# Optimization experiments

Hardware: AMD Instinct MI355X
Metric: run time of the kernel (lower is better)

## Reference

```python
import jax, jax.numpy as jnp
import numpy as np

B, D, T = 8, 1024, 512
HID, NH, NL = 256, 4, 2
OUT = HID // NH  # 64 per-head dim
ALPHA = 0.2      # leaky relu slope
EPS = 1e-5       # layernorm eps


def setup_inputs() -> dict:
    key = jax.random.key(0)
    ks = jax.random.split(key, 10)
    X_obs = jax.random.normal(ks[0], (B, D, T), dtype=jnp.float32)
    mask = (jax.random.uniform(ks[1], (B, D, T)) < 0.8).astype(jnp.float32)
    W_in = jax.random.normal(ks[2], (2 * T, HID), dtype=jnp.float32) * (1.0 / np.sqrt(2 * T))
    b_in = jnp.zeros((HID,), dtype=jnp.float32)
    gat_W = jax.random.normal(ks[3], (NL, NH, HID, OUT), dtype=jnp.float32) * (1.0 / np.sqrt(HID))
    gat_a = jax.random.normal(ks[4], (NL, NH, 2 * OUT), dtype=jnp.float32) * 0.1
    ln_g = jnp.ones((NL, HID), dtype=jnp.float32)
    ln_b = jnp.zeros((NL, HID), dtype=jnp.float32)
    W_out = jax.random.normal(ks[5], (HID, T), dtype=jnp.float32) * (1.0 / np.sqrt(HID))
    b_out = jnp.zeros((T,), dtype=jnp.float32)
    return dict(X_obs=X_obs, mask=mask, W_in=W_in, b_in=b_in, gat_W=gat_W,
                gat_a=gat_a, ln_g=ln_g, ln_b=ln_b, W_out=W_out, b_out=b_out)


def _layer_norm(x, g, b):
    mu = jnp.mean(x, axis=-1, keepdims=True)
    var = jnp.mean((x - mu) ** 2, axis=-1, keepdims=True)
    return (x - mu) * jax.lax.rsqrt(var + EPS) * g + b


def _gat_forward(X_obs, mask, W_in, b_in, gat_W, gat_a, ln_g, ln_b, W_out, b_out):
    # mean-impute per (d, t) position across batch
    obs_sum = jnp.sum(X_obs * mask, axis=0, keepdims=True)
    obs_cnt = jnp.sum(mask, axis=0, keepdims=True)
    pos_mean = obs_sum / (obs_cnt + 1e-10)
    X_mean = X_obs * mask + (1.0 - mask) * pos_mean

    x = jnp.concatenate([X_mean, mask], axis=-1)       # (B, D, 2T)
    h = x @ W_in + b_in                                 # (B, N, HID)

    for l in range(NL):
        Wl = gat_W[l]                                   # (H, HID, OUT)
        a_left = gat_a[l, :, :OUT]                      # (H, OUT)
        a_right = gat_a[l, :, OUT:]                     # (H, OUT)
        hW = jnp.einsum('bnd,hde->bhne', h, Wl)         # (B, H, N, OUT)
        # e_ij = leakyrelu(a_left . h_i + a_right . h_j) -- avoids O(N^2 * 2d) concat
        s_l = jnp.einsum('bhne,he->bhn', hW, a_left)
        s_r = jnp.einsum('bhne,he->bhn', hW, a_right)
        e = jax.nn.leaky_relu(s_l[..., :, None] + s_r[..., None, :], ALPHA)  # (B,H,N,N)
        attn = jax.nn.softmax(e, axis=-1)
        head_out = jnp.einsum('bhnm,bhme->bhne', attn, hW)                   # (B,H,N,OUT)
        h_new = jnp.transpose(head_out, (0, 2, 1, 3)).reshape(h.shape[0], h.shape[1], HID)
        h = _layer_norm(h + h_new, ln_g[l], ln_b[l])

    return h @ W_out + b_out                            # (B, D, T)


def reference(X_obs, mask, W_in, b_in, gat_W, gat_a, ln_g, ln_b, W_out, b_out):
    return _gat_forward(X_obs, mask, W_in, b_in, gat_W, gat_a, ln_g, ln_b, W_out, b_out)
```

## Files before the change

### kernel.cpp

```cpp
#include <hip/hip_runtime.h>
#include <hip/hip_bf16.h>

constexpr int B_   = 8;
constexpr int D_   = 1024;
constexpr int T_   = 512;
constexpr int HID_ = 256;
constexpr int NH_  = 4;
constexpr int NL_  = 2;
constexpr float ALPHA_ = 0.2f;
constexpr float EPS_   = 1e-5f;
constexpr int OUT_ = 64;
constexpr int M_ = B_ * D_;
constexpr int DT_ = D_ * T_;
constexpr int KIN_ = 2 * T_;
constexpr int CKS_ = 132;
constexpr int NCH_ = 32;
constexpr int CR_  = 32;

typedef __attribute__((ext_vector_type(8))) short short8;
typedef __attribute__((ext_vector_type(4))) float floatx4;

__device__ __forceinline__ unsigned short f2bf(float f) {
    unsigned int u = __float_as_uint(f);
    unsigned int r = u + 0x7fffu + ((u >> 16) & 1u);
    return (unsigned short)(r >> 16);
}
__device__ __forceinline__ float bf2f(unsigned short u) {
    return __uint_as_float(((unsigned int)u) << 16);
}
__device__ __forceinline__ unsigned int kenc(float f) {
    unsigned int u = __float_as_uint(f);
    return (u & 0x80000000u) ? ~u : (u | 0x80000000u);
}
__device__ __forceinline__ float kdec(unsigned int k) {
    unsigned int u = (k & 0x80000000u) ? (k ^ 0x80000000u) : ~k;
    return __uint_as_float(u);
}

__global__ __launch_bounds__(256) void prep_k(const float* __restrict__ X,
                                              const float* __restrict__ Mk,
                                              const float* __restrict__ W_in,
                                              const float* __restrict__ gatW,
                                              const float* __restrict__ W_out,
                                              unsigned short* __restrict__ Ain,
                                              unsigned short* __restrict__ Wt_in,
                                              unsigned short* __restrict__ Wcat,
                                              unsigned short* __restrict__ WtO,
                                              unsigned int* __restrict__ rmaxkey) {
    int bx = blockIdx.x;
    if (bx < 512) {
        int idx4 = (bx * 256 + threadIdx.x) * 4;
        int t = idx4 & (T_ - 1);
        int d = idx4 >> 9;
        float4 x[B_], m[B_];
        float4 s = {0, 0, 0, 0}, c = {0, 0, 0, 0};
#pragma unroll
        for (int b = 0; b < B_; b++) {
            x[b] = *(const float4*)&X[(size_t)b * DT_ + idx4];
            m[b] = *(const float4*)&Mk[(size_t)b * DT_ + idx4];
            s.x += x[b].x * m[b].x; s.y += x[b].y * m[b].y;
            s.z += x[b].z * m[b].z; s.w += x[b].w * m[b].w;
            c.x += m[b].x; c.y += m[b].y; c.z += m[b].z; c.w += m[b].w;
        }
        float4 pm;
        pm.x = s.x / (c.x + 1e-10f); pm.y = s.y / (c.y + 1e-10f);
        pm.z = s.z / (c.z + 1e-10f); pm.w = s.w / (c.w + 1e-10f);
#pragma unroll
        for (int b = 0; b < B_; b++) {
            size_t row = (size_t)b * D_ + d;
            ushort4 xm, mk;
            xm.x = f2bf(x[b].x * m[b].x + (1.f - m[b].x) * pm.x);
            xm.y = f2bf(x[b].y * m[b].y + (1.f - m[b].y) * pm.y);
            xm.z = f2bf(x[b].z * m[b].z + (1.f - m[b].z) * pm.z);
            xm.w = f2bf(x[b].w * m[b].w + (1.f - m[b].w) * pm.w);
            mk.x = f2bf(m[b].x); mk.y = f2bf(m[b].y);
            mk.z = f2bf(m[b].z); mk.w = f2bf(m[b].w);
            *(ushort4*)&Ain[row * KIN_ + t]      = xm;
            *(ushort4*)&Ain[row * KIN_ + T_ + t] = mk;
        }
    } else {
        int idx = (bx - 512) * 256 + threadIdx.x;
        if (idx < 64) rmaxkey[idx] = 0u;
        if (idx < 262144) {
            int n = idx >> 10, k = idx & 1023;
            Wt_in[idx] = f2bf(W_in[(size_t)k * HID_ + n]);
        } else if (idx < 393216) {
            int j = idx - 262144;
            int l = j >> 16, n = (j >> 8) & 255, k = j & 255;
            int h = n >> 6, e = n & 63;
            Wcat[j] = f2bf(gatW[(((size_t)(l * NH_ + h) * HID_) + k) * OUT_ + e]);
        } else {
            int j = idx - 393216;
            int n = j >> 8, k = j & 255;
            WtO[j] = f2bf(W_out[(size_t)k * T_ + n]);
        }
    }
}

template <int MODE>
__global__ __launch_bounds__(256) void gemm_bf16_k(
        const unsigned short* __restrict__ A,
        const unsigned short* __restrict__ Bt,
        const float* __restrict__ bias,
        float* __restrict__ C,
        unsigned short* __restrict__ Cb,
        const float* __restrict__ ga,
        float* __restrict__ s_l,
        float* __restrict__ s_r,
        unsigned int* __restrict__ rmaxkey,
        int Nsz, int Ksz) {
    __shared__ __align__(16) unsigned short As[2][64 * 72];
    __shared__ __align__(16) unsigned short Bs[2][64 * 72];
    int tid = threadIdx.x;
    int wave = tid >> 6, lane = tid & 63;
    int q = lane >> 4, r16 = lane & 15;
    int rowbase = blockIdx.y * 64;
    int colbase = blockIdx.x * 64;

    int srow = tid >> 3, sk = (tid & 7) * 8;
    const unsigned short* Ap0 = A + (size_t)(rowbase + srow) * Ksz + sk;
    const unsigned short* Ap1 = A + (size_t)(rowbase + srow + 32) * Ksz + sk;
    const unsigned short* Bp0 = Bt + (size_t)(colbase + srow) * Ksz + sk;
    const unsigned short* Bp1 = Bt + (size_t)(colbase + srow + 32) * Ksz + sk;
    int la0 = srow * 72 + sk, la1 = (srow + 32) * 72 + sk;

    floatx4 acc[4];
#pragma unroll
    for (int i = 0; i < 4; i++) acc[i] = (floatx4)0.f;

    uint4 pa0 = *(const uint4*)Ap0, pa1 = *(const uint4*)Ap1;
    uint4 pb0 = *(const uint4*)Bp0, pb1 = *(const uint4*)Bp1;
    *(uint4*)&As[0][la0] = pa0;
    *(uint4*)&As[0][la1] = pa1;
    *(uint4*)&Bs[0][la0] = pb0;
    *(uint4*)&Bs[0][la1] = pb1;

    int nk = Ksz >> 6;
    for (int it = 0; it < nk; it++) {
        int cur = it & 1;
        __syncthreads();
        if (it + 1 < nk) {
            int kt = (it + 1) << 6;
            pa0 = *(const uint4*)(Ap0 + kt);
            pa1 = *(const uint4*)(Ap1 + kt);
            pb0 = *(const uint4*)(Bp0 + kt);
            pb1 = *(const uint4*)(Bp1 + kt);
        }
#pragma unroll
        for (int t = 0; t < 2; t++) {
            short8 a = *(const short8*)&As[cur][(wave * 16 + r16) * 72 + t * 32 + q * 8];
#pragma unroll
            for (int ni = 0; ni < 4; ni++) {
                short8 b = *(const short8*)&Bs[cur][(ni * 16 + r16) * 72 + t * 32 + q * 8];
                acc[ni] = __builtin_amdgcn_mfma_f32_16x16x32_bf16(a, b, acc[ni], 0, 0, 0);
            }
        }
        if (it + 1 < nk) {
            int nxt = cur ^ 1;
            *(uint4*)&As[nxt][la0] = pa0;
            *(uint4*)&As[nxt][la1] = pa1;
            *(uint4*)&Bs[nxt][la0] = pb0;
            *(uint4*)&Bs[nxt][la1] = pb1;
        }
    }
    if constexpr (MODE == 2) {
        int bhh = ((rowbase >> 10) << 2) + blockIdx.x;
        int nb0 = rowbase & (D_ - 1);
        int nb = nb0 + wave * 16;
        const float* gab = ga + blockIdx.x * 2 * OUT_;
        float al4[4], ar4[4];
#pragma unroll
        for (int ni = 0; ni < 4; ni++) {
            al4[ni] = gab[ni * 16 + r16];
            ar4[ni] = gab[OUT_ + ni * 16 + r16];
        }
        float slv[4], srv[4];
#pragma unroll
        for (int rr = 0; rr < 4; rr++) {
            float s1 = 0.f, s2 = 0.f;
#pragma unroll
            for (int ni = 0; ni < 4; ni++) {
                s1 += acc[ni][rr] * al4[ni];
                s2 += acc[ni][rr] * ar4[ni];
            }
            slv[rr] = s1;
            srv[rr] = s2;
        }
#pragma unroll
        for (int off = 1; off < 16; off <<= 1) {
#pragma unroll
            for (int rr = 0; rr < 4; rr++) {
                slv[rr] += __shfl_xor(slv[rr], off, 64);
                srv[rr] += __shfl_xor(srv[rr], off, 64);
            }
        }
        {
            int rsel = r16 & 3;
            float sv = (rsel == 0) ? slv[0] : (rsel == 1) ? slv[1] : (rsel == 2) ? slv[2] : slv[3];
            float rv = (rsel == 0) ? srv[0] : (rsel == 1) ? srv[1] : (rsel == 2) ? srv[2] : srv[3];
            int n = nb + q * 4 + rsel;
            if (r16 < 4)                 s_l[bhh * D_ + n] = sv;
            else if (r16 >= 8 && r16 < 12) s_r[bhh * D_ + n] = rv;
        }
        float mx = fmaxf(fmaxf(srv[0], srv[1]), fmaxf(srv[2], srv[3]));
        mx = fmaxf(mx, __shfl_xor(mx, 16, 64));
        mx = fmaxf(mx, __shfl_xor(mx, 32, 64));
        if (lane == 0) atomicMax(&rmaxkey[bhh], kenc(mx));
        __syncthreads();
        unsigned short* st = &As[0][0];
#pragma unroll
        for (int ni = 0; ni < 4; ni++)
#pragma unroll
            for (int rr = 0; rr < 4; rr++)
                st[(wave * 16 + q * 4 + rr) * 72 + ni * 16 + r16] = f2bf(acc[ni][rr]);
        __syncthreads();
#pragma unroll
        for (int i = 0; i < 2; i++) {
            int idx = tid * 2 + i;
            int row = idx >> 3, seg = idx & 7;
            uint4 v = *(const uint4*)&st[row * 72 + seg * 8];
            *(uint4*)&Cb[((size_t)bhh << 16) + ((size_t)(nb0 + row) << 6) + seg * 8] = v;
        }
    } else {
#pragma unroll
        for (int rr = 0; rr < 4; rr++) {
            int row = rowbase + wave * 16 + q * 4 + rr;
#pragma unroll
            for (int ni = 0; ni < 4; ni++) {
                int col = colbase + ni * 16 + r16;
                float v = acc[ni][rr] + (bias ? bias[col] : 0.f);
                C[(size_t)row * Nsz + col] = v;
                if constexpr (MODE == 1) Cb[(size_t)row * Nsz + col] = f2bf(v);
            }
        }
    }
}

__global__ __launch_bounds__(1024) void rank_k(
        const float* __restrict__ sr_g,
        const unsigned int* __restrict__ rmaxkey,
        float* __restrict__ srt,
        int* __restrict__ sig,
        float* __restrict__ wm) {
    __shared__ float skey[1024];
    __shared__ short part[16][64];
    int bh = blockIdx.x, seg = blockIdx.y;
    int tid = threadIdx.x;
    skey[tid] = sr_g[bh * D_ + tid];
    __syncthreads();
    int lane = tid & 63, wv = tid >> 6;
    int el = seg * 64 + lane;
    float k = skey[el];
    int m0 = wv * 64;
    int cnt = 0;
#pragma unroll 4
    for (int m = m0; m < m0 + 64; ++m) {
        float km = skey[m];
        cnt += (km < k) || (km == k && m < el);
    }
    part[wv][lane] = (short)cnt;
    __syncthreads();
    if (tid < 64) {
        int rank = 0;
#pragma unroll
        for (int w = 0; w < 16; ++w) rank += part[w][tid];
        int elg = seg * 64 + tid;
        float key = skey[elg];
        float rm = kdec(rmaxkey[bh]);
        float u = key - rm;
        float w1 = __expf(u), w2 = __expf(ALPHA_ * u);
        srt[bh * D_ + rank] = key;
        sig[bh * D_ + rank] = elg;
        *(float2*)&wm[(size_t)(bh * D_ + rank) * 2] = float2{w1, w2};
    }
}

__global__ __launch_bounds__(64) void chunksum_k(
        const unsigned short* __restrict__ hwN,
        const int* __restrict__ sig,
        const float* __restrict__ wm,
        float* __restrict__ csum,
        float* __restrict__ csca) {
    int bh = blockIdx.x, c = blockIdx.y;
    int e = threadIdx.x;
    const unsigned short* vb = hwN + ((size_t)bh << 16);
    int t0 = c * CR_;
    float a1 = 0.f, a2 = 0.f, q1 = 0.f, q2 = 0.f;
#pragma unroll 4
    for (int t = t0; t < t0 + CR_; ++t) {
        float2 ww = *(const float2*)&wm[(size_t)(bh * D_ + t) * 2];
        float v = bf2f(vb[((size_t)sig[bh * D_ + t] << 6) + e]);
        a1 = fmaf(ww.x, v, a1);
        a2 = fmaf(ww.y, v, a2);
        q1 += ww.x; q2 += ww.y;
    }
    *(float2*)&csum[(((size_t)bh * NCH_ + c) * 64 + e) * 2] = float2{a1, a2};
    if (e == 0) *(float2*)&csca[((size_t)bh * NCH_ + c) * 2] = float2{q1, q2};
}

__global__ __launch_bounds__(64) void ckwrite_k(
        const unsigned short* __restrict__ hwN,
        const int* __restrict__ sig,
        const float* __restrict__ wm,
        const float* __restrict__ csum,
        const float* __restrict__ csca,
        float* __restrict__ ck) {
    int bh = blockIdx.x, c = blockIdx.y;
    int e = threadIdx.x;
    float r1 = 0.f, r2 = 0.f, p1 = 0.f, p2 = 0.f;
    for (int cc = 0; cc < c; ++cc) {
        float2 s  = *(const float2*)&csum[(((size_t)bh * NCH_ + cc) * 64 + e) * 2];
        float2 sc = *(const float2*)&csca[((size_t)bh * NCH_ + cc) * 2];
        r1 += s.x; r2 += s.y;
        p1 += sc.x; p2 += sc.y;
    }
    const unsigned short* vb = hwN + ((size_t)bh << 16);
    float* ckb = ck + (size_t)bh * 1025 * CKS_;
    int t0 = c * CR_;
    for (int t = t0; t < t0 + CR_; ++t) {
        *(float2*)&ckb[(size_t)t * CKS_ + 2 * e] = float2{r1, r2};
        if (e == 0) *(float2*)&ckb[(size_t)t * CKS_ + 128] = float2{p1, p2};
        float2 ww = *(const float2*)&wm[(size_t)(bh * D_ + t) * 2];
        float v = bf2f(vb[((size_t)sig[bh * D_ + t] << 6) + e]);
        r1 = fmaf(ww.x, v, r1);
        r2 = fmaf(ww.y, v, r2);
        p1 += ww.x; p2 += ww.y;
    }
    if (c == NCH_ - 1) {
        *(float2*)&ckb[(size_t)1024 * CKS_ + 2 * e] = float2{r1, r2};
        if (e == 0) *(float2*)&ckb[(size_t)1024 * CKS_ + 128] = float2{p1, p2};
    }
}

__global__ __launch_bounds__(512) void rowln_k(
        float* __restrict__ h,
        const float* __restrict__ sl_g,
        const unsigned int* __restrict__ rmaxkey,
        const float* __restrict__ srt,
        const float* __restrict__ ck,
        const float* __restrict__ g,
        const float* __restrict__ bb,
        unsigned short* __restrict__ hbf) {
    __shared__ float srtL[4][1024];
    __shared__ float hnew[32][260];
    __shared__ float ckT1[4][64];
    __shared__ float qTs[4][2];
    __shared__ float pdF[128][2];
    __shared__ int   pdT[128];
    int blk = blockIdx.x;
    int b = blk >> 5;
    int d0 = (blk & 31) << 5;
    int tid = threadIdx.x;
    for (int i = tid; i < 4096; i += 512)
        srtL[i >> 10][i & 1023] = srt[(size_t)((b * 4 + (i >> 10)) * D_) + (i & 1023)];
    if (tid < 256) {
        int hh = tid >> 6, e = tid & 63;
        ckT1[hh][e] = ck[((size_t)((b * 4 + hh) * 1025 + 1024)) * CKS_ + 2 * e];
    }
    if (tid < 8) {
        int hh = tid >> 1;
        qTs[hh][tid & 1] = ck[((size_t)((b * 4 + hh) * 1025 + 1024)) * CKS_ + 128 + (tid & 1)];
    }
    __syncthreads();
    if (tid < 128) {
        int r = tid & 31, h4 = tid >> 5;
        int bh = b * 4 + h4;
        float sl = sl_g[bh * D_ + d0 + r];
        float rm = kdec(rmaxkey[bh]);
        float x = sl + rm;
        float Mn = fmaxf(x, ALPHA_ * x);
        float A  = __expf(x - Mn);
        float B2 = __expf(ALPHA_ * x - Mn);
        float key = -sl;
        int lo = 0, hi = 1024;
        while (lo < hi) {
            int mid = (lo + hi) >> 1;
            if (srtL[h4][mid] < key) lo = mid + 1; else hi = mid;
        }
        float2 qs = *(const float2*)&ck[((size_t)(bh * 1025 + lo)) * CKS_ + 128];
        float den = A * (qTs[h4][0] - qs.x) + B2 * qs.y;
        float inv = 1.f / den;
        pdF[tid][0] = A * inv;
        pdF[tid][1] = B2 * inv;
        pdT[tid] = lo;
    }
    __syncthreads();
    int wv = tid >> 6, e = tid & 63;
    for (int p = wv; p < 128; p += 8) {
        int r = p & 31, h4 = p >> 5;
        int bh = b * 4 + h4;
        float fA = pdF[p][0], fB = pdF[p][1];
        int t = pdT[p];
        float2 P = *(const float2*)&ck[((size_t)(bh * 1025 + t)) * CKS_ + 2 * e];
        hnew[r][h4 * 64 + e] = fA * (ckT1[h4][e] - P.x) + fB * P.y;
    }
    __syncthreads();
    for (int rr = wv * 4; rr < wv * 4 + 4; ++rr) {
        size_t grow = ((((size_t)b << 10) + d0 + rr) << 8);
        float4 a  = *(const float4*)&h[grow + e * 4];
        float4 nv = *(const float4*)&hnew[rr][e * 4];
        float4 v = {a.x + nv.x, a.y + nv.y, a.z + nv.z, a.w + nv.w};
        float s = v.x + v.y + v.z + v.w;
#pragma unroll
        for (int off = 1; off < 64; off <<= 1) s += __shfl_xor(s, off, 64);
        float mu = s * (1.f / HID_);
        float4 dd = {v.x - mu, v.y - mu, v.z - mu, v.w - mu};
        float s2 = dd.x * dd.x + dd.y * dd.y + dd.z * dd.z + dd.w * dd.w;
#pragma unroll
        for (int off = 1; off < 64; off <<= 1) s2 += __shfl_xor(s2, off, 64);
        float rs = rsqrtf(s2 * (1.f / HID_) + EPS_);
        float4 gg = *(const float4*)&g[e * 4];
        float4 bv = *(const float4*)&bb[e * 4];
        float4 res;
        res.x = dd.x * rs * gg.x + bv.x;
        res.y = dd.y * rs * gg.y + bv.y;
        res.z = dd.z * rs * gg.z + bv.z;
        res.w = dd.w * rs * gg.w + bv.w;
        *(float4*)&h[grow + e * 4] = res;
        ushort4 pk = {f2bf(res.x), f2bf(res.y), f2bf(res.z), f2bf(res.w)};
        *(ushort4*)&hbf[grow + e * 4] = pk;
    }
}

extern "C" void kernel_launch(void* const* d_in, const int* in_sizes, int n_in,
                              void* d_out, int out_size, void* d_ws, size_t ws_size,
                              hipStream_t stream) {
    const float* X_obs = (const float*)d_in[0];
    const float* mask  = (const float*)d_in[1];
    const float* W_in  = (const float*)d_in[2];
    const float* b_in  = (const float*)d_in[3];
    const float* gat_W = (const float*)d_in[4];
    const float* gat_a = (const float*)d_in[5];
    const float* ln_g  = (const float*)d_in[6];
    const float* ln_b  = (const float*)d_in[7];
    const float* W_out = (const float*)d_in[8];
    const float* b_out = (const float*)d_in[9];
    float* out = (float*)d_out;

    char* base = (char*)d_ws;
    unsigned short* Ain = (unsigned short*)base;
    unsigned short* hwN = (unsigned short*)base;
    float* ck   = (float*)(base + (4u << 20));
    float* csum = (float*)(base + (21u << 20));
    float* csca = (float*)(base + (21u << 20) + (512u << 10));
    float* wm   = (float*)(base + (22u << 20));
    float* srtb = (float*)(base + (22u << 20) + (512u << 10));
    int*   sig  = (int*)(base + (22u << 20) + (768u << 10));
    float* hbuf = (float*)(base + (23u << 20));
    unsigned short* hbf   = (unsigned short*)(base + (31u << 20));
    unsigned short* Wt_in = (unsigned short*)(base + (35u << 20));
    unsigned short* Wcat  = Wt_in + (size_t)HID_ * KIN_;
    unsigned short* WtO   = Wcat + (size_t)NL_ * HID_ * HID_;
    float* slb = (float*)(WtO + (size_t)T_ * HID_);
    float* srb = slb + B_ * NH_ * D_;
    unsigned int* rmaxkey = (unsigned int*)(srb + B_ * NH_ * D_);

    prep_k<<<2560, 256, 0, stream>>>(X_obs, mask, W_in, gat_W, W_out,
                                     Ain, Wt_in, Wcat, WtO, rmaxkey);

    gemm_bf16_k<1><<<dim3(HID_ / 64, M_ / 64), 256, 0, stream>>>(
        Ain, Wt_in, b_in, hbuf, hbf, nullptr, nullptr, nullptr, nullptr,
        HID_, KIN_);

    for (int l = 0; l < NL_; l++) {
        gemm_bf16_k<2><<<dim3(HID_ / 64, M_ / 64), 256, 0, stream>>>(
            hbf, Wcat + (size_t)l * HID_ * HID_, nullptr, nullptr, hwN,
            gat_a + (size_t)l * NH_ * 2 * OUT_, slb, srb, rmaxkey + l * 32,
            HID_, HID_);
        rank_k<<<dim3(32, 16), 1024, 0, stream>>>(srb, rmaxkey + l * 32,
                                                  srtb, sig, wm);
        chunksum_k<<<dim3(32, NCH_), 64, 0, stream>>>(hwN, sig, wm, csum, csca);
        ckwrite_k<<<dim3(32, NCH_), 64, 0, stream>>>(hwN, sig, wm, csum, csca, ck);
        rowln_k<<<256, 512, 0, stream>>>(hbuf, slb, rmaxkey + l * 32,
                                         srtb, ck,
                                         ln_g + (size_t)l * HID_,
                                         ln_b + (size_t)l * HID_, hbf);
    }

    gemm_bf16_k<0><<<dim3(T_ / 64, M_ / 64), 256, 0, stream>>>(
        hbf, WtO, b_out, out, nullptr, nullptr, nullptr, nullptr, nullptr,
        T_, HID_);
}
```

Baseline: 249.2 us.

## Fuse all stages into one persistent kernel with software grid barriers

Replaces the sequence of separate launches (prep, input GEMM, per-layer GAT GEMM, rank, chunk-sum, prefix write, row layernorm, output GEMM) with one persistent 512-block kernel. Stages are separated by atomic grid barriers, and each stage's work is remapped onto the fixed block grid. The chunking is also re-split into 64 chunks of 16 rows. This aims to remove launch gaps and tail effects between many small kernels. In exchange it depends on all 512 blocks being co-resident, and some stages now run with fewer threads per block than before.

```diff
diff --git a/kernel.cpp b/kernel.cpp
--- a/kernel.cpp
+++ b/kernel.cpp
@@ -14,8 +14,9 @@
 constexpr int DT_ = D_ * T_;
 constexpr int KIN_ = 2 * T_;
 constexpr int CKS_ = 132;
-constexpr int NCH_ = 32;
-constexpr int CR_  = 32;
+constexpr int NCH_ = 64;
+constexpr int CR_  = 16;
+constexpr int NB_  = 512;
 
 typedef __attribute__((ext_vector_type(8))) short short8;
 typedef __attribute__((ext_vector_type(4))) float floatx4;
@@ -37,19 +38,192 @@
     return __uint_as_float(u);
 }
 
-__global__ __launch_bounds__(256) void prep_k(const float* __restrict__ X,
-                                              const float* __restrict__ Mk,
-                                              const float* __restrict__ W_in,
-                                              const float* __restrict__ gatW,
-                                              const float* __restrict__ W_out,
-                                              unsigned short* __restrict__ Ain,
-                                              unsigned short* __restrict__ Wt_in,
-                                              unsigned short* __restrict__ Wcat,
-                                              unsigned short* __restrict__ WtO,
-                                              unsigned int* __restrict__ rmaxkey) {
-    int bx = blockIdx.x;
-    if (bx < 512) {
-        int idx4 = (bx * 256 + threadIdx.x) * 4;
+__device__ __forceinline__ void gridbar(unsigned int* bar) {
+    __syncthreads();
+    if (threadIdx.x == 0) {
+        __threadfence();
+        atomicAdd(bar, 1u);
+        while (__hip_atomic_load(bar, __ATOMIC_ACQUIRE, __HIP_MEMORY_SCOPE_AGENT)
+               < (unsigned)NB_)
+            __builtin_amdgcn_s_sleep(2);
+    }
+    __syncthreads();
+}
+
+__global__ __launch_bounds__(256) void init_k(unsigned int* __restrict__ bar) {
+    if (threadIdx.x < 64) bar[threadIdx.x] = 0u;
+}
+
+struct GemmSm {
+    unsigned short As[2][64 * 72];
+    unsigned short Bs[2][64 * 72];
+};
+
+template <int MODE>
+__device__ void gemm_tile(
+        const unsigned short* __restrict__ A,
+        const unsigned short* __restrict__ Bt,
+        const float* __restrict__ bias,
+        float* __restrict__ C,
+        unsigned short* __restrict__ Cb,
+        const float* __restrict__ ga,
+        float* __restrict__ s_l,
+        float* __restrict__ s_r,
+        unsigned int* __restrict__ rmaxkey,
+        int Nsz, int Ksz, int bx, int by, GemmSm& sm) {
+    __syncthreads();
+    int tid = threadIdx.x;
+    int wave = tid >> 6, lane = tid & 63;
+    int q = lane >> 4, r16 = lane & 15;
+    int rowbase = by * 64;
+    int colbase = bx * 64;
+
+    int srow = tid >> 3, sk = (tid & 7) * 8;
+    const unsigned short* Ap0 = A + (size_t)(rowbase + srow) * Ksz + sk;
+    const unsigned short* Ap1 = A + (size_t)(rowbase + srow + 32) * Ksz + sk;
+    const unsigned short* Bp0 = Bt + (size_t)(colbase + srow) * Ksz + sk;
+    const unsigned short* Bp1 = Bt + (size_t)(colbase + srow + 32) * Ksz + sk;
+    int la0 = srow * 72 + sk, la1 = (srow + 32) * 72 + sk;
+
+    floatx4 acc[4];
+#pragma unroll
+    for (int i = 0; i < 4; i++) acc[i] = (floatx4)0.f;
+
+    uint4 pa0 = *(const uint4*)Ap0, pa1 = *(const uint4*)Ap1;
+    uint4 pb0 = *(const uint4*)Bp0, pb1 = *(const uint4*)Bp1;
+    *(uint4*)&sm.As[0][la0] = pa0;
+    *(uint4*)&sm.As[0][la1] = pa1;
+    *(uint4*)&sm.Bs[0][la0] = pb0;
+    *(uint4*)&sm.Bs[0][la1] = pb1;
+
+    int nk = Ksz >> 6;
+    for (int it = 0; it < nk; it++) {
+        int cur = it & 1;
+        __syncthreads();
+        if (it + 1 < nk) {
+            int kt = (it + 1) << 6;
+            pa0 = *(const uint4*)(Ap0 + kt);
+            pa1 = *(const uint4*)(Ap1 + kt);
+            pb0 = *(const uint4*)(Bp0 + kt);
+            pb1 = *(const uint4*)(Bp1 + kt);
+        }
+#pragma unroll
+        for (int t = 0; t < 2; t++) {
+            short8 a = *(const short8*)&sm.As[cur][(wave * 16 + r16) * 72 + t * 32 + q * 8];
+#pragma unroll
+            for (int ni = 0; ni < 4; ni++) {
+                short8 b = *(const short8*)&sm.Bs[cur][(ni * 16 + r16) * 72 + t * 32 + q * 8];
+                acc[ni] = __builtin_amdgcn_mfma_f32_16x16x32_bf16(a, b, acc[ni], 0, 0, 0);
+            }
+        }
+        if (it + 1 < nk) {
+            int nxt = cur ^ 1;
+            *(uint4*)&sm.As[nxt][la0] = pa0;
+            *(uint4*)&sm.As[nxt][la1] = pa1;
+            *(uint4*)&sm.Bs[nxt][la0] = pb0;
+            *(uint4*)&sm.Bs[nxt][la1] = pb1;
+        }
+    }
+    if constexpr (MODE == 2) {
+        int bhh = ((rowbase >> 10) << 2) + bx;
+        int nb0 = rowbase & (D_ - 1);
+        int nb = nb0 + wave * 16;
+        const float* gab = ga + bx * 2 * OUT_;
+        float al4[4], ar4[4];
+#pragma unroll
+        for (int ni = 0; ni < 4; ni++) {
+            al4[ni] = gab[ni * 16 + r16];
+            ar4[ni] = gab[OUT_ + ni * 16 + r16];
+        }
+        float slv[4], srv[4];
+#pragma unroll
+        for (int rr = 0; rr < 4; rr++) {
+            float s1 = 0.f, s2 = 0.f;
+#pragma unroll
+            for (int ni = 0; ni < 4; ni++) {
+                s1 += acc[ni][rr] * al4[ni];
+                s2 += acc[ni][rr] * ar4[ni];
+            }
+            slv[rr] = s1;
+            srv[rr] = s2;
+        }
+#pragma unroll
+        for (int off = 1; off < 16; off <<= 1) {
+#pragma unroll
+            for (int rr = 0; rr < 4; rr++) {
+                slv[rr] += __shfl_xor(slv[rr], off, 64);
+                srv[rr] += __shfl_xor(srv[rr], off, 64);
+            }
+        }
+        {
+            int rsel = r16 & 3;
+            float sv = (rsel == 0) ? slv[0] : (rsel == 1) ? slv[1] : (rsel == 2) ? slv[2] : slv[3];
+            float rv = (rsel == 0) ? srv[0] : (rsel == 1) ? srv[1] : (rsel == 2) ? srv[2] : srv[3];
+            int n = nb + q * 4 + rsel;
+            if (r16 < 4)                 s_l[bhh * D_ + n] = sv;
+            else if (r16 >= 8 && r16 < 12) s_r[bhh * D_ + n] = rv;
+        }
+        float mx = fmaxf(fmaxf(srv[0], srv[1]), fmaxf(srv[2], srv[3]));
+        mx = fmaxf(mx, __shfl_xor(mx, 16, 64));
+        mx = fmaxf(mx, __shfl_xor(mx, 32, 64));
+        if (lane == 0) atomicMax(&rmaxkey[bhh], kenc(mx));
+        __syncthreads();
+        unsigned short* st = &sm.As[0][0];
+#pragma unroll
+        for (int ni = 0; ni < 4; ni++)
+#pragma unroll
+            for (int rr = 0; rr < 4; rr++)
+                st[(wave * 16 + q * 4 + rr) * 72 + ni * 16 + r16] = f2bf(acc[ni][rr]);
+        __syncthreads();
+#pragma unroll
+        for (int i = 0; i < 2; i++) {
+            int idx = tid * 2 + i;
+            int row = idx >> 3, seg = idx & 7;
+            uint4 v = *(const uint4*)&st[row * 72 + seg * 8];
+            *(uint4*)&Cb[((size_t)bhh << 16) + ((size_t)(nb0 + row) << 6) + seg * 8] = v;
+        }
+    } else {
+#pragma unroll
+        for (int rr = 0; rr < 4; rr++) {
+            int row = rowbase + wave * 16 + q * 4 + rr;
+#pragma unroll
+            for (int ni = 0; ni < 4; ni++) {
+                int col = colbase + ni * 16 + r16;
+                float v = acc[ni][rr] + (bias ? bias[col] : 0.f);
+                C[(size_t)row * Nsz + col] = v;
+                if constexpr (MODE == 1) Cb[(size_t)row * Nsz + col] = f2bf(v);
+            }
+        }
+    }
+}
+
+__global__ __launch_bounds__(256, 2) void mega_k(
+        const float* __restrict__ X, const float* __restrict__ Mk,
+        const float* __restrict__ W_in, const float* __restrict__ b_in,
+        const float* __restrict__ gatW, const float* __restrict__ gat_a,
+        const float* __restrict__ ln_g, const float* __restrict__ ln_b,
+        const float* __restrict__ W_out, const float* __restrict__ b_out,
+        float* __restrict__ out,
+        unsigned short* __restrict__ Ain, unsigned short* __restrict__ hwN,
+        float* __restrict__ ck, float* __restrict__ csum, float* __restrict__ csca,
+        float* __restrict__ wm, float* __restrict__ srtb, int* __restrict__ sig,
+        float* __restrict__ hbuf, unsigned short* __restrict__ hbf,
+        unsigned short* __restrict__ Wt_in, unsigned short* __restrict__ Wcat,
+        unsigned short* __restrict__ WtO,
+        float* __restrict__ slb, float* __restrict__ srb,
+        unsigned int* __restrict__ rmaxkey, unsigned int* __restrict__ bar) {
+    __shared__ union {
+        GemmSm g;
+        struct { float skey[1024]; short part[4][64]; } rk;
+        struct { float srtL[4][1024]; float hnew[16][260];
+                 float ckT1[4][64]; float qTs[4][2];
+                 float pdF[64][2]; int pdT[64]; } rl;
+    } sm;
+    const int blk = blockIdx.x, tid = threadIdx.x;
+    const int gtid = blk * 256 + tid;
+
+    {
+        int idx4 = gtid * 4;
         int t = idx4 & (T_ - 1);
         int d = idx4 >> 9;
         float4 x[B_], m[B_];
@@ -78,347 +252,203 @@
             *(ushort4*)&Ain[row * KIN_ + t]      = xm;
             *(ushort4*)&Ain[row * KIN_ + T_ + t] = mk;
         }
-    } else {
-        int idx = (bx - 512) * 256 + threadIdx.x;
-        if (idx < 64) rmaxkey[idx] = 0u;
-        if (idx < 262144) {
-            int n = idx >> 10, k = idx & 1023;
-            Wt_in[idx] = f2bf(W_in[(size_t)k * HID_ + n]);
-        } else if (idx < 393216) {
-            int j = idx - 262144;
-            int l = j >> 16, n = (j >> 8) & 255, k = j & 255;
-            int h = n >> 6, e = n & 63;
-            Wcat[j] = f2bf(gatW[(((size_t)(l * NH_ + h) * HID_) + k) * OUT_ + e]);
-        } else {
-            int j = idx - 393216;
-            int n = j >> 8, k = j & 255;
-            WtO[j] = f2bf(W_out[(size_t)k * T_ + n]);
-        }
-    }
-}
-
-template <int MODE>
-__global__ __launch_bounds__(256) void gemm_bf16_k(
-        const unsigned short* __restrict__ A,
-        const unsigned short* __restrict__ Bt,
-        const float* __restrict__ bias,
-        float* __restrict__ C,
-        unsigned short* __restrict__ Cb,
-        const float* __restrict__ ga,
-        float* __restrict__ s_l,
-        float* __restrict__ s_r,
-        unsigned int* __restrict__ rmaxkey,
-        int Nsz, int Ksz) {
-    __shared__ __align__(16) unsigned short As[2][64 * 72];
-    __shared__ __align__(16) unsigned short Bs[2][64 * 72];
-    int tid = threadIdx.x;
-    int wave = tid >> 6, lane = tid & 63;
-    int q = lane >> 4, r16 = lane & 15;
-    int rowbase = blockIdx.y * 64;
-    int colbase = blockIdx.x * 64;
-
-    int srow = tid >> 3, sk = (tid & 7) * 8;
-    const unsigned short* Ap0 = A + (size_t)(rowbase + srow) * Ksz + sk;
-    const unsigned short* Ap1 = A + (size_t)(rowbase + srow + 32) * Ksz + sk;
-    const unsigned short* Bp0 = Bt + (size_t)(colbase + srow) * Ksz + sk;
-    const unsigned short* Bp1 = Bt + (size_t)(colbase + srow + 32) * Ksz + sk;
-    int la0 = srow * 72 + sk, la1 = (srow + 32) * 72 + sk;
-
-    floatx4 acc[4];
-#pragma unroll
-    for (int i = 0; i < 4; i++) acc[i] = (floatx4)0.f;
-
-    uint4 pa0 = *(const uint4*)Ap0, pa1 = *(const uint4*)Ap1;
-    uint4 pb0 = *(const uint4*)Bp0, pb1 = *(const uint4*)Bp1;
-    *(uint4*)&As[0][la0] = pa0;
-    *(uint4*)&As[0][la1] = pa1;
-    *(uint4*)&Bs[0][la0] = pb0;
-    *(uint4*)&Bs[0][la1] = pb1;
-
-    int nk = Ksz >> 6;
-    for (int it = 0; it < nk; it++) {
-        int cur = it & 1;
-        __syncthreads();
-        if (it + 1 < nk) {
-            int kt = (it + 1) << 6;
-            pa0 = *(const uint4*)(Ap0 + kt);
-            pa1 = *(const uint4*)(Ap1 + kt);
-            pb0 = *(const uint4*)(Bp0 + kt);
-            pb1 = *(const uint4*)(Bp1 + kt);
-        }
-#pragma unroll
-        for (int t = 0; t < 2; t++) {
-            short8 a = *(const short8*)&As[cur][(wave * 16 + r16) * 72 + t * 32 + q * 8];
-#pragma unroll
-            for (int ni = 0; ni < 4; ni++) {
-                short8 b = *(const short8*)&Bs[cur][(ni * 16 + r16) * 72 + t * 32 + q * 8];
-                acc[ni] = __builtin_amdgcn_mfma_f32_16x16x32_bf16(a, b, acc[ni], 0, 0, 0);
-            }
-        }
-        if (it + 1 < nk) {
-            int nxt = cur ^ 1;
-            *(uint4*)&As[nxt][la0] = pa0;
-            *(uint4*)&As[nxt][la1] = pa1;
-            *(uint4*)&Bs[nxt][la0] = pb0;
-            *(uint4*)&Bs[nxt][la1] = pb1;
-        }
-    }
-    if constexpr (MODE == 2) {
-        int bhh = ((rowbase >> 10) << 2) + blockIdx.x;
-        int nb0 = rowbase & (D_ - 1);
-        int nb = nb0 + wave * 16;
-        const float* gab = ga + blockIdx.x * 2 * OUT_;
-        float al4[4], ar4[4];
-#pragma unroll
-        for (int ni = 0; ni < 4; ni++) {
-            al4[ni] = gab[ni * 16 + r16];
-            ar4[ni] = gab[OUT_ + ni * 16 + r16];
-        }
-        float slv[4], srv[4];
-#pragma unroll
-        for (int rr = 0; rr < 4; rr++) {
-            float s1 = 0.f, s2 = 0.f;
-#pragma unroll
-            for (int ni = 0; ni < 4; ni++) {
-                s1 += acc[ni][rr] * al4[ni];
-                s2 += acc[ni][rr] * ar4[ni];
-            }
-            slv[rr] = s1;
-            srv[rr] = s2;
-        }
-#pragma unroll
-        for (int off = 1; off < 16; off <<= 1) {
-#pragma unroll
-            for (int rr = 0; rr < 4; rr++) {
-                slv[rr] += __shfl_xor(slv[rr], off, 64);
-                srv[rr] += __shfl_xor(srv[rr], off, 64);
-            }
-        }
+#pragma unroll
+        for (int k4 = 0; k4 < 4; ++k4) {
+            int idx = gtid + k4 * 131072;
+            if (idx < 64) rmaxkey[idx] = 0u;
+            if (idx < 262144) {
+                int n = idx >> 10, k = idx & 1023;
+                Wt_in[idx] = f2bf(W_in[(size_t)k * HID_ + n]);
+            } else if (idx < 393216) {
+                int j = idx - 262144;
+                int l = j >> 16, n = (j >> 8) & 255, k = j & 255;
+                int h = n >> 6, e = n & 63;
+                Wcat[j] = f2bf(gatW[(((size_t)(l * NH_ + h) * HID_) + k) * OUT_ + e]);
+            } else {
+                int j = idx - 393216;
+                int n = j >> 8, k = j & 255;
+                WtO[j] = f2bf(W_out[(size_t)k * T_ + n]);
+            }
+        }
+    }
+    int bi = 0;
+    gridbar(&bar[bi++]);
+    gemm_tile<1>(Ain, Wt_in, b_in, hbuf, hbf, nullptr, nullptr, nullptr, nullptr,
+                 HID_, KIN_, blk & 3, blk >> 2, sm.g);
+
+    for (int l = 0; l < NL_; ++l) {
+        unsigned int* rmxl = rmaxkey + l * 32;
+        gridbar(&bar[bi++]);
+        gemm_tile<2>(hbf, Wcat + (size_t)l * HID_ * HID_, nullptr, nullptr, hwN,
+                     gat_a + (size_t)l * NH_ * 2 * OUT_, slb, srb, rmxl,
+                     HID_, HID_, blk & 3, blk >> 2, sm.g);
+        gridbar(&bar[bi++]);
         {
-            int rsel = r16 & 3;
-            float sv = (rsel == 0) ? slv[0] : (rsel == 1) ? slv[1] : (rsel == 2) ? slv[2] : slv[3];
-            float rv = (rsel == 0) ? srv[0] : (rsel == 1) ? srv[1] : (rsel == 2) ? srv[2] : srv[3];
-            int n = nb + q * 4 + rsel;
-            if (r16 < 4)                 s_l[bhh * D_ + n] = sv;
-            else if (r16 >= 8 && r16 < 12) s_r[bhh * D_ + n] = rv;
-        }
-        float mx = fmaxf(fmaxf(srv[0], srv[1]), fmaxf(srv[2], srv[3]));
-        mx = fmaxf(mx, __shfl_xor(mx, 16, 64));
-        mx = fmaxf(mx, __shfl_xor(mx, 32, 64));
-        if (lane == 0) atomicMax(&rmaxkey[bhh], kenc(mx));
-        __syncthreads();
-        unsigned short* st = &As[0][0];
-#pragma unroll
-        for (int ni = 0; ni < 4; ni++)
-#pragma unroll
-            for (int rr = 0; rr < 4; rr++)
-                st[(wave * 16 + q * 4 + rr) * 72 + ni * 16 + r16] = f2bf(acc[ni][rr]);
-        __syncthreads();
-#pragma unroll
-        for (int i = 0; i < 2; i++) {
-            int idx = tid * 2 + i;
-            int row = idx >> 3, seg = idx & 7;
-            uint4 v = *(const uint4*)&st[row * 72 + seg * 8];
-            *(uint4*)&Cb[((size_t)bhh << 16) + ((size_t)(nb0 + row) << 6) + seg * 8] = v;
-        }
-    } else {
-#pragma unroll
-        for (int rr = 0; rr < 4; rr++) {
-            int row = rowbase + wave * 16 + q * 4 + rr;
-#pragma unroll
-            for (int ni = 0; ni < 4; ni++) {
-                int col = colbase + ni * 16 + r16;
-                float v = acc[ni][rr] + (bias ? bias[col] : 0.f);
-                C[(size_t)row * Nsz + col] = v;
-                if constexpr (MODE == 1) Cb[(size_t)row * Nsz + col] = f2bf(v);
-            }
-        }
-    }
-}
-
-__global__ __launch_bounds__(1024) void rank_k(
-        const float* __restrict__ sr_g,
-        const unsigned int* __restrict__ rmaxkey,
-        float* __restrict__ srt,
-        int* __restrict__ sig,
-        float* __restrict__ wm) {
-    __shared__ float skey[1024];
-    __shared__ short part[16][64];
-    int bh = blockIdx.x, seg = blockIdx.y;
-    int tid = threadIdx.x;
-    skey[tid] = sr_g[bh * D_ + tid];
-    __syncthreads();
-    int lane = tid & 63, wv = tid >> 6;
-    int el = seg * 64 + lane;
-    float k = skey[el];
-    int m0 = wv * 64;
-    int cnt = 0;
+            int bh = blk >> 4, seg = blk & 15;
+            *(float4*)&sm.rk.skey[tid * 4] = *(const float4*)&srb[bh * D_ + tid * 4];
+            __syncthreads();
+            int lane = tid & 63, w4 = tid >> 6;
+            int el = seg * 64 + lane;
+            float key = sm.rk.skey[el];
+            int cnt = 0;
 #pragma unroll 4
-    for (int m = m0; m < m0 + 64; ++m) {
-        float km = skey[m];
-        cnt += (km < k) || (km == k && m < el);
-    }
-    part[wv][lane] = (short)cnt;
-    __syncthreads();
-    if (tid < 64) {
-        int rank = 0;
-#pragma unroll
-        for (int w = 0; w < 16; ++w) rank += part[w][tid];
-        int elg = seg * 64 + tid;
-        float key = skey[elg];
-        float rm = kdec(rmaxkey[bh]);
-        float u = key - rm;
-        float w1 = __expf(u), w2 = __expf(ALPHA_ * u);
-        srt[bh * D_ + rank] = key;
-        sig[bh * D_ + rank] = elg;
-        *(float2*)&wm[(size_t)(bh * D_ + rank) * 2] = float2{w1, w2};
-    }
-}
-
-__global__ __launch_bounds__(64) void chunksum_k(
-        const unsigned short* __restrict__ hwN,
-        const int* __restrict__ sig,
-        const float* __restrict__ wm,
-        float* __restrict__ csum,
-        float* __restrict__ csca) {
-    int bh = blockIdx.x, c = blockIdx.y;
-    int e = threadIdx.x;
-    const unsigned short* vb = hwN + ((size_t)bh << 16);
-    int t0 = c * CR_;
-    float a1 = 0.f, a2 = 0.f, q1 = 0.f, q2 = 0.f;
+            for (int m = w4 * 256; m < w4 * 256 + 256; ++m) {
+                float km = sm.rk.skey[m];
+                cnt += (km < key) || (km == key && m < el);
+            }
+            sm.rk.part[w4][lane] = (short)cnt;
+            __syncthreads();
+            if (tid < 64) {
+                int rank = sm.rk.part[0][tid] + sm.rk.part[1][tid] +
+                           sm.rk.part[2][tid] + sm.rk.part[3][tid];
+                int elg = seg * 64 + tid;
+                float kk = sm.rk.skey[elg];
+                float rm = kdec(rmxl[bh]);
+                float u = kk - rm;
+                srtb[bh * D_ + rank] = kk;
+                sig[bh * D_ + rank] = elg;
+                *(float2*)&wm[(size_t)(bh * D_ + rank) * 2] =
+                    float2{__expf(u), __expf(ALPHA_ * u)};
+            }
+        }
+        gridbar(&bar[bi++]);
+        {
+            int gwv = gtid >> 6;
+            int bh = gwv >> 6, c = gwv & 63;
+            int e = tid & 63;
+            const unsigned short* vb = hwN + ((size_t)bh << 16);
+            int t0 = c * CR_;
+            float a1 = 0.f, a2 = 0.f, q1 = 0.f, q2 = 0.f;
 #pragma unroll 4
-    for (int t = t0; t < t0 + CR_; ++t) {
-        float2 ww = *(const float2*)&wm[(size_t)(bh * D_ + t) * 2];
-        float v = bf2f(vb[((size_t)sig[bh * D_ + t] << 6) + e]);
-        a1 = fmaf(ww.x, v, a1);
-        a2 = fmaf(ww.y, v, a2);
-        q1 += ww.x; q2 += ww.y;
-    }
-    *(float2*)&csum[(((size_t)bh * NCH_ + c) * 64 + e) * 2] = float2{a1, a2};
-    if (e == 0) *(float2*)&csca[((size_t)bh * NCH_ + c) * 2] = float2{q1, q2};
-}
-
-__global__ __launch_bounds__(64) void ckwrite_k(
-        const unsigned short* __restrict__ hwN,
-        const int* __restrict__ sig,
-        const float* __restrict__ wm,
-        const float* __restrict__ csum,
-        const float* __restrict__ csca,
-        float* __restrict__ ck) {
-    int bh = blockIdx.x, c = blockIdx.y;
-    int e = threadIdx.x;
-    float r1 = 0.f, r2 = 0.f, p1 = 0.f, p2 = 0.f;
-    for (int cc = 0; cc < c; ++cc) {
-        float2 s  = *(const float2*)&csum[(((size_t)bh * NCH_ + cc) * 64 + e) * 2];
-        float2 sc = *(const float2*)&csca[((size_t)bh * NCH_ + cc) * 2];
-        r1 += s.x; r2 += s.y;
-        p1 += sc.x; p2 += sc.y;
-    }
-    const unsigned short* vb = hwN + ((size_t)bh << 16);
-    float* ckb = ck + (size_t)bh * 1025 * CKS_;
-    int t0 = c * CR_;
-    for (int t = t0; t < t0 + CR_; ++t) {
-        *(float2*)&ckb[(size_t)t * CKS_ + 2 * e] = float2{r1, r2};
-        if (e == 0) *(float2*)&ckb[(size_t)t * CKS_ + 128] = float2{p1, p2};
-        float2 ww = *(const float2*)&wm[(size_t)(bh * D_ + t) * 2];
-        float v = bf2f(vb[((size_t)sig[bh * D_ + t] << 6) + e]);
-        r1 = fmaf(ww.x, v, r1);
-        r2 = fmaf(ww.y, v, r2);
-        p1 += ww.x; p2 += ww.y;
-    }
-    if (c == NCH_ - 1) {
-        *(float2*)&ckb[(size_t)1024 * CKS_ + 2 * e] = float2{r1, r2};
-        if (e == 0) *(float2*)&ckb[(size_t)1024 * CKS_ + 128] = float2{p1, p2};
-    }
-}
-
-__global__ __launch_bounds__(512) void rowln_k(
-        float* __restrict__ h,
-        const float* __restrict__ sl_g,
-        const unsigned int* __restrict__ rmaxkey,
-        const float* __restrict__ srt,
-        const float* __restrict__ ck,
-        const float* __restrict__ g,
-        const float* __restrict__ bb,
-        unsigned short* __restrict__ hbf) {
-    __shared__ float srtL[4][1024];
-    __shared__ float hnew[32][260];
-    __shared__ float ckT1[4][64];
-    __shared__ float qTs[4][2];
-    __shared__ float pdF[128][2];
-    __shared__ int   pdT[128];
-    int blk = blockIdx.x;
-    int b = blk >> 5;
-    int d0 = (blk & 31) << 5;
-    int tid = threadIdx.x;
-    for (int i = tid; i < 4096; i += 512)
-        srtL[i >> 10][i & 1023] = srt[(size_t)((b * 4 + (i >> 10)) * D_) + (i & 1023)];
-    if (tid < 256) {
-        int hh = tid >> 6, e = tid & 63;
-        ckT1[hh][e] = ck[((size_t)((b * 4 + hh) * 1025 + 1024)) * CKS_ + 2 * e];
-    }
-    if (tid < 8) {
-        int hh = tid >> 1;
-        qTs[hh][tid & 1] = ck[((size_t)((b * 4 + hh) * 1025 + 1024)) * CKS_ + 128 + (tid & 1)];
-    }
-    __syncthreads();
-    if (tid < 128) {
-        int r = tid & 31, h4 = tid >> 5;
-        int bh = b * 4 + h4;
-        float sl = sl_g[bh * D_ + d0 + r];
-        float rm = kdec(rmaxkey[bh]);
-        float x = sl + rm;
-        float Mn = fmaxf(x, ALPHA_ * x);
-        float A  = __expf(x - Mn);
-        float B2 = __expf(ALPHA_ * x - Mn);
-        float key = -sl;
-        int lo = 0, hi = 1024;
-        while (lo < hi) {
-            int mid = (lo + hi) >> 1;
-            if (srtL[h4][mid] < key) lo = mid + 1; else hi = mid;
-        }
-        float2 qs = *(const float2*)&ck[((size_t)(bh * 1025 + lo)) * CKS_ + 128];
-        float den = A * (qTs[h4][0] - qs.x) + B2 * qs.y;
-        float inv = 1.f / den;
-        pdF[tid][0] = A * inv;
-        pdF[tid][1] = B2 * inv;
-        pdT[tid] = lo;
-    }
-    __syncthreads();
-    int wv = tid >> 6, e = tid & 63;
-    for (int p = wv; p < 128; p += 8) {
-        int r = p & 31, h4 = p >> 5;
-        int bh = b * 4 + h4;
-        float fA = pdF[p][0], fB = pdF[p][1];
-        int t = pdT[p];
-        float2 P = *(const float2*)&ck[((size_t)(bh * 1025 + t)) * CKS_ + 2 * e];
-        hnew[r][h4 * 64 + e] = fA * (ckT1[h4][e] - P.x) + fB * P.y;
-    }
-    __syncthreads();
-    for (int rr = wv * 4; rr < wv * 4 + 4; ++rr) {
-        size_t grow = ((((size_t)b << 10) + d0 + rr) << 8);
-        float4 a  = *(const float4*)&h[grow + e * 4];
-        float4 nv = *(const float4*)&hnew[rr][e * 4];
-        float4 v = {a.x + nv.x, a.y + nv.y, a.z + nv.z, a.w + nv.w};
-        float s = v.x + v.y + v.z + v.w;
-#pragma unroll
-        for (int off = 1; off < 64; off <<= 1) s += __shfl_xor(s, off, 64);
-        float mu = s * (1.f / HID_);
-        float4 dd = {v.x - mu, v.y - mu, v.z - mu, v.w - mu};
-        float s2 = dd.x * dd.x + dd.y * dd.y + dd.z * dd.z + dd.w * dd.w;
-#pragma unroll
-        for (int off = 1; off < 64; off <<= 1) s2 += __shfl_xor(s2, off, 64);
-        float rs = rsqrtf(s2 * (1.f / HID_) + EPS_);
-        float4 gg = *(const float4*)&g[e * 4];
-        float4 bv = *(const float4*)&bb[e * 4];
-        float4 res;
-        res.x = dd.x * rs * gg.x + bv.x;
-        res.y = dd.y * rs * gg.y + bv.y;
-        res.z = dd.z * rs * gg.z + bv.z;
-        res.w = dd.w * rs * gg.w + bv.w;
-        *(float4*)&h[grow + e * 4] = res;
-        ushort4 pk = {f2bf(res.x), f2bf(res.y), f2bf(res.z), f2bf(res.w)};
-        *(ushort4*)&hbf[grow + e * 4] = pk;
+            for (int t = t0; t < t0 + CR_; ++t) {
+                float2 ww = *(const float2*)&wm[(size_t)(bh * D_ + t) * 2];
+                float v = bf2f(vb[((size_t)sig[bh * D_ + t] << 6) + e]);
+                a1 = fmaf(ww.x, v, a1);
+                a2 = fmaf(ww.y, v, a2);
+                q1 += ww.x; q2 += ww.y;
+            }
+            *(float2*)&csum[(((size_t)bh * NCH_ + c) * 64 + e) * 2] = float2{a1, a2};
+            if (e == 0) *(float2*)&csca[((size_t)bh * NCH_ + c) * 2] = float2{q1, q2};
+        }
+        gridbar(&bar[bi++]);
+        {
+            int gwv = gtid >> 6;
+            int bh = gwv >> 6, c = gwv & 63;
+            int e = tid & 63;
+            float r1 = 0.f, r2 = 0.f, p1 = 0.f, p2 = 0.f;
+            for (int cc = 0; cc < c; ++cc) {
+                float2 s2 = *(const float2*)&csum[(((size_t)bh * NCH_ + cc) * 64 + e) * 2];
+                float2 sc = *(const float2*)&csca[((size_t)bh * NCH_ + cc) * 2];
+                r1 += s2.x; r2 += s2.y;
+                p1 += sc.x; p2 += sc.y;
+            }
+            const unsigned short* vb = hwN + ((size_t)bh << 16);
+            float* ckb = ck + (size_t)bh * 1025 * CKS_;
+            int t0 = c * CR_;
+            for (int t = t0; t < t0 + CR_; ++t) {
+                *(float2*)&ckb[(size_t)t * CKS_ + 2 * e] = float2{r1, r2};
+                if (e == 0) *(float2*)&ckb[(size_t)t * CKS_ + 128] = float2{p1, p2};
+                float2 ww = *(const float2*)&wm[(size_t)(bh * D_ + t) * 2];
+                float v = bf2f(vb[((size_t)sig[bh * D_ + t] << 6) + e]);
+                r1 = fmaf(ww.x, v, r1);
+                r2 = fmaf(ww.y, v, r2);
+                p1 += ww.x; p2 += ww.y;
+            }
+            if (c == NCH_ - 1) {
+                *(float2*)&ckb[(size_t)1024 * CKS_ + 2 * e] = float2{r1, r2};
+                if (e == 0) *(float2*)&ckb[(size_t)1024 * CKS_ + 128] = float2{p1, p2};
+            }
+        }
+        gridbar(&bar[bi++]);
+        {
+            int b = blk >> 6;
+            int d0 = (blk & 63) << 4;
+            for (int i = tid; i < 1024; i += 256) {
+#pragma unroll
+                for (int hh = 0; hh < 4; ++hh)
+                    sm.rl.srtL[hh][i] = srtb[(size_t)(b * 4 + hh) * D_ + i];
+            }
+            {
+                int hh = tid >> 6, e = tid & 63;
+                sm.rl.ckT1[hh][e] =
+                    ck[((size_t)((b * 4 + hh) * 1025 + 1024)) * CKS_ + 2 * e];
+            }
+            if (tid < 8) {
+                int hh = tid >> 1;
+                sm.rl.qTs[hh][tid & 1] =
+                    ck[((size_t)((b * 4 + hh) * 1025 + 1024)) * CKS_ + 128 + (tid & 1)];
+            }
+            __syncthreads();
+            if (tid < 64) {
+                int r = tid & 15, h4 = tid >> 4;
+                int bh = b * 4 + h4;
+                float sl = slb[bh * D_ + d0 + r];
+                float rm = kdec(rmxl[bh]);
+                float x = sl + rm;
+                float Mn = fmaxf(x, ALPHA_ * x);
+                float A  = __expf(x - Mn);
+                float B2 = __expf(ALPHA_ * x - Mn);
+                float key = -sl;
+                int lo = 0, hi = 1024;
+                while (lo < hi) {
+                    int mid = (lo + hi) >> 1;
+                    if (sm.rl.srtL[h4][mid] < key) lo = mid + 1; else hi = mid;
+                }
+                float2 qs = *(const float2*)&ck[((size_t)(bh * 1025 + lo)) * CKS_ + 128];
+                float den = A * (sm.rl.qTs[h4][0] - qs.x) + B2 * qs.y;
+                float inv = 1.f / den;
+                sm.rl.pdF[tid][0] = A * inv;
+                sm.rl.pdF[tid][1] = B2 * inv;
+                sm.rl.pdT[tid] = lo;
+            }
+            __syncthreads();
+            int w4 = tid >> 6, e = tid & 63;
+            for (int p = w4; p < 64; p += 4) {
+                int r = p & 15, h4 = p >> 4;
+                int bh = b * 4 + h4;
+                float2 P = *(const float2*)
+                    &ck[((size_t)(bh * 1025 + sm.rl.pdT[p])) * CKS_ + 2 * e];
+                sm.rl.hnew[r][h4 * 64 + e] =
+                    sm.rl.pdF[p][0] * (sm.rl.ckT1[h4][e] - P.x) + sm.rl.pdF[p][1] * P.y;
+            }
+            __syncthreads();
+            const float* g  = ln_g + (size_t)l * HID_;
+            const float* bb = ln_b + (size_t)l * HID_;
+#pragma unroll
+            for (int j = 0; j < 4; ++j) {
+                int rr = w4 * 4 + j;
+                size_t grow = (((size_t)b << 10) + d0 + rr) << 8;
+                float4 a  = *(const float4*)&hbuf[grow + e * 4];
+                float4 nv = *(const float4*)&sm.rl.hnew[rr][e * 4];
+                float4 v = {a.x + nv.x, a.y + nv.y, a.z + nv.z, a.w + nv.w};
+                float s = v.x + v.y + v.z + v.w;
+#pragma unroll
+                for (int off = 1; off < 64; off <<= 1) s += __shfl_xor(s, off, 64);
+                float mu = s * (1.f / HID_);
+                float4 dd = {v.x - mu, v.y - mu, v.z - mu, v.w - mu};
+                float s2 = dd.x * dd.x + dd.y * dd.y + dd.z * dd.z + dd.w * dd.w;
+#pragma unroll
+                for (int off = 1; off < 64; off <<= 1) s2 += __shfl_xor(s2, off, 64);
+                float rs = rsqrtf(s2 * (1.f / HID_) + EPS_);
+                float4 gg  = *(const float4*)&g[e * 4];
+                float4 bv  = *(const float4*)&bb[e * 4];
+                float4 res;
+                res.x = dd.x * rs * gg.x + bv.x;
+                res.y = dd.y * rs * gg.y + bv.y;
+                res.z = dd.z * rs * gg.z + bv.z;
+                res.w = dd.w * rs * gg.w + bv.w;
+                *(float4*)&hbuf[grow + e * 4] = res;
+                ushort4 pk = {f2bf(res.x), f2bf(res.y), f2bf(res.z), f2bf(res.w)};
+                *(ushort4*)&hbf[grow + e * 4] = pk;
+            }
+        }
+    }
+    gridbar(&bar[bi++]);
+#pragma unroll
+    for (int k = 0; k < 2; ++k) {
+        int tt = blk * 2 + k;
+        gemm_tile<0>(hbf, WtO, b_out, out, nullptr, nullptr, nullptr, nullptr,
+                     nullptr, T_, HID_, tt & 7, tt >> 3, sm.g);
     }
 }
 
@@ -441,8 +471,8 @@
     unsigned short* Ain = (unsigned short*)base;
     unsigned short* hwN = (unsigned short*)base;
     float* ck   = (float*)(base + (4u << 20));
+    float* csca = (float*)(base + (20u << 20) + (768u << 10));
     float* csum = (float*)(base + (21u << 20));
-    float* csca = (float*)(base + (21u << 20) + (512u << 10));
     float* wm   = (float*)(base + (22u << 20));
     float* srtb = (float*)(base + (22u << 20) + (512u << 10));
     int*   sig  = (int*)(base + (22u << 20) + (768u << 10));
@@ -454,30 +484,12 @@
     float* slb = (float*)(WtO + (size_t)T_ * HID_);
     float* srb = slb + B_ * NH_ * D_;
     unsigned int* rmaxkey = (unsigned int*)(srb + B_ * NH_ * D_);
-
-    prep_k<<<2560, 256, 0, stream>>>(X_obs, mask, W_in, gat_W, W_out,
-                                     Ain, Wt_in, Wcat, WtO, rmaxkey);
-
-    gemm_bf16_k<1><<<dim3(HID_ / 64, M_ / 64), 256, 0, stream>>>(
-        Ain, Wt_in, b_in, hbuf, hbf, nullptr, nullptr, nullptr, nullptr,
-        HID_, KIN_);
-
-    for (int l = 0; l < NL_; l++) {
-        gemm_bf16_k<2><<<dim3(HID_ / 64, M_ / 64), 256, 0, stream>>>(
-            hbf, Wcat + (size_t)l * HID_ * HID_, nullptr, nullptr, hwN,
-            gat_a + (size_t)l * NH_ * 2 * OUT_, slb, srb, rmaxkey + l * 32,
-            HID_, HID_);
-        rank_k<<<dim3(32, 16), 1024, 0, stream>>>(srb, rmaxkey + l * 32,
-                                                  srtb, sig, wm);
-        chunksum_k<<<dim3(32, NCH_), 64, 0, stream>>>(hwN, sig, wm, csum, csca);
-        ckwrite_k<<<dim3(32, NCH_), 64, 0, stream>>>(hwN, sig, wm, csum, csca, ck);
-        rowln_k<<<256, 512, 0, stream>>>(hbuf, slb, rmaxkey + l * 32,
-                                         srtb, ck,
-                                         ln_g + (size_t)l * HID_,
-                                         ln_b + (size_t)l * HID_, hbf);
-    }
-
-    gemm_bf16_k<0><<<dim3(T_ / 64, M_ / 64), 256, 0, stream>>>(
-        hbf, WtO, b_out, out, nullptr, nullptr, nullptr, nullptr, nullptr,
-        T_, HID_);
-}
+    unsigned int* bar = (unsigned int*)(base + (40u << 20));
+
+    init_k<<<1, 256, 0, stream>>>(bar);
+    mega_k<<<NB_, 256, 0, stream>>>(X_obs, mask, W_in, b_in, gat_W, gat_a,
+                                    ln_g, ln_b, W_out, b_out, out,
+                                    Ain, hwN, ck, csum, csca, wm, srtb, sig,
+                                    hbuf, hbf, Wt_in, Wcat, WtO,
+                                    slb, srb, rmaxkey, bar);
+}
```

Result: slower. 990.9 us (+297.6%).
